# Kernel optimization log

Measured on AMD Instinct MI355X. Metric: run time of the kernel, lower is better.

Reference implementation:

```python
import jax, jax.numpy as jnp
import numpy as np

B, S, D, H = 2, 2048, 1024, 16
DK = D // H


def setup_inputs() -> dict:
    key = jax.random.key(0)
    ks = jax.random.split(key, 8)
    q = jax.random.normal(ks[0], (B, S, D), dtype=jnp.float32)
    k = jax.random.normal(ks[1], (B, S, D), dtype=jnp.float32)
    v = jax.random.normal(ks[2], (B, S, D), dtype=jnp.float32)
    mask = jax.random.randint(ks[3], (B, 1, S, S), 0, 2, dtype=jnp.int32)
    sc = 1.0 / np.sqrt(D)
    Wq = jax.random.normal(ks[4], (D, D), dtype=jnp.float32) * sc
    Wk = jax.random.normal(ks[5], (D, D), dtype=jnp.float32) * sc
    Wv = jax.random.normal(ks[6], (D, D), dtype=jnp.float32) * sc
    Wo = jax.random.normal(ks[7], (D, D), dtype=jnp.float32) * sc
    return {"q": q, "k": k, "v": v, "mask": mask, "Wq": Wq, "Wk": Wk, "Wv": Wv, "Wo": Wo}


def reference(q, k, v, mask, Wq, Wk, Wv, Wo):
    # Linear projections (torch Linear: x @ W.T; bias=False). Weights here stored
    # as [D, D] applied as x @ W (equivalent parameterization).
    query = q @ Wq  # [B,S,D]
    key = k @ Wk
    value = v @ Wv
    # split heads -> [B,H,S,DK]
    query = query.reshape(B, S, H, DK).transpose(0, 2, 1, 3)
    key = key.reshape(B, S, H, DK).transpose(0, 2, 1, 3)
    value = value.reshape(B, S, H, DK).transpose(0, 2, 1, 3)
    scores = jnp.einsum('bhqd,bhkd->bhqk', query, key) / jnp.sqrt(jnp.float32(DK))
    scores = jnp.where(mask == 0, jnp.float32(-1e9), scores)
    probs = jax.nn.softmax(scores, axis=-1)  # dropout p=0.0 -> identity
    x = jnp.einsum('bhqk,bhkd->bhqd', probs, value)
    x = x.transpose(0, 2, 1, 3).reshape(B, S, D)
    return x @ Wo
```

## Files before the change

### kernel.cpp

```cpp
#include <hip/hip_runtime.h>
#include <hip/hip_bf16.h>
#include <math.h>

#define B_ 2
#define S_ 2048
#define D_ 1024
#define H_ 16
#define DK_ 64
#define SW_ (S_ / 64)

typedef unsigned short u16;
typedef unsigned int u32;
typedef unsigned long long u64;
typedef __attribute__((ext_vector_type(8))) short short8;
typedef __attribute__((ext_vector_type(4))) float float4_;
typedef __attribute__((ext_vector_type(4))) unsigned int uint4_;

static __device__ inline u16 f_to_bf16(float f) {
    union { float f; u32 i; } x; x.f = f;
    u32 r = x.i + 0x7fff + ((x.i >> 16) & 1);
    return (u16)(r >> 16);
}

static __device__ __forceinline__ u32 cvtpk(float a, float b) {
    u32 r;
    asm("v_cvt_pk_bf16_f32 %0, %1, %2" : "=v"(r) : "v"(a), "v"(b));
    return r;
}

static __device__ __forceinline__ float fast_exp2(float x) {
#if __has_builtin(__builtin_amdgcn_exp2f)
    return __builtin_amdgcn_exp2f(x);
#else
    return exp2f(x);
#endif
}

static __device__ inline void gl_lds16(const u16* g, u16* l) {
    __builtin_amdgcn_global_load_lds((const __attribute__((address_space(1))) void*)g,
                                     (__attribute__((address_space(3))) void*)l, 16, 0, 0);
}

__global__ __launch_bounds__(256) void prep(const float* __restrict__ q,
                                            const float* __restrict__ k,
                                            const float* __restrict__ v,
                                            const int* __restrict__ mask,
                                            const float* __restrict__ W0,
                                            const float* __restrict__ W1,
                                            const float* __restrict__ W2,
                                            const float* __restrict__ W3,
                                            u16* __restrict__ qb, u16* __restrict__ kb,
                                            u16* __restrict__ vb,
                                            u16* __restrict__ T0, u16* __restrict__ T1,
                                            u16* __restrict__ T2, u16* __restrict__ T3,
                                            u64* __restrict__ mpk) {
    __shared__ float tile[32][33];
    int gx = blockIdx.x, tid = threadIdx.x;
    if (gx < 6144) {
        int z = gx >> 11;
        int bx = gx & 2047;
        const float* s = (z == 0) ? q : ((z == 1) ? k : v);
        u16* d = (z == 0) ? qb : ((z == 1) ? kb : vb);
        int i = (bx * 256 + tid) * 8;
        #pragma unroll
        for (int j = 0; j < 8; ++j) d[i + j] = f_to_bf16(s[i + j]);
    } else if (gx < 10240) {
        int g2 = gx - 6144;
        int z = g2 >> 10;
        int rem = g2 & 1023;
        const float* W = (z == 0) ? W0 : ((z == 1) ? W1 : ((z == 2) ? W2 : W3));
        u16* Wt = (z == 0) ? T0 : ((z == 1) ? T1 : ((z == 2) ? T2 : T3));
        int k0 = (rem >> 5) * 32, n0 = (rem & 31) * 32;
        int tx = tid & 31, ty = tid >> 5;
        #pragma unroll
        for (int i2 = 0; i2 < 4; ++i2) {
            int row = ty + i2 * 8;
            tile[row][tx] = W[(size_t)(k0 + row) * D_ + n0 + tx];
        }
        __syncthreads();
        #pragma unroll
        for (int i2 = 0; i2 < 4; ++i2) {
            int row = ty + i2 * 8;
            Wt[(size_t)(n0 + row) * D_ + k0 + tx] = f_to_bf16(tile[tx][row]);
        }
    } else {
        int g3 = gx - 10240;
        int wv = (g3 * 256 + tid) >> 6;
        int lane = tid & 63;
        #pragma unroll
        for (int i2 = 0; i2 < 8; ++i2) {
            int wd = wv * 8 + i2;
            u64 bits = __ballot(mask[(size_t)wd * 64 + lane] != 0);
            if (lane == 0) mpk[wd] = bits;
        }
    }
}

static __device__ __forceinline__ void gemm128_body(u16* lds,
                                                    const u16* __restrict__ A,
                                                    const u16* __restrict__ Bt,
                                                    int K, float4_ (&acc)[4][4]) {
    u16* ldsA = lds;
    u16* ldsB = lds + 8192;
    int tm = blockIdx.x, tn = blockIdx.y;
    int t = threadIdx.x, l = t & 63;
    int w = t >> 6, wr = w >> 1, wc = w & 1;
    int colL = l & 15, grp = l >> 4;
    int sw4 = (grp ^ ((colL >> 1) & 3)) << 3;
    int f0 = t, f1 = t + 256;
    int row0 = f0 >> 2, kc0 = (((f0 & 3) ^ ((f0 >> 3) & 3)) << 3);
    int row1 = f1 >> 2, kc1 = (((f1 & 3) ^ ((f1 >> 3) & 3)) << 3);
    const u16* gA0 = A  + (size_t)(tm * 128 + row0) * K + kc0;
    const u16* gA1 = A  + (size_t)(tm * 128 + row1) * K + kc1;
    const u16* gB0 = Bt + (size_t)(tn * 128 + row0) * K + kc0;
    const u16* gB1 = Bt + (size_t)(tn * 128 + row1) * K + kc1;

    #pragma unroll
    for (int mi = 0; mi < 4; ++mi)
        #pragma unroll
        for (int ni = 0; ni < 4; ++ni)
            acc[mi][ni] = (float4_){0.f, 0.f, 0.f, 0.f};

    gl_lds16(gA0, ldsA + f0 * 8);
    gl_lds16(gA1, ldsA + f1 * 8);
    gl_lds16(gB0, ldsB + f0 * 8);
    gl_lds16(gB1, ldsB + f1 * 8);

    for (int k0 = 0; k0 < K; k0 += 32) {
        int cur = (k0 >> 5) & 1;
        if (k0 + 32 < K) {
            int nb = (cur ^ 1) * 4096;
            gl_lds16(gA0 + k0 + 32, ldsA + nb + f0 * 8);
            gl_lds16(gA1 + k0 + 32, ldsA + nb + f1 * 8);
            gl_lds16(gB0 + k0 + 32, ldsB + nb + f0 * 8);
            gl_lds16(gB1 + k0 + 32, ldsB + nb + f1 * 8);
            asm volatile("s_waitcnt vmcnt(4)" ::: "memory");
        } else {
            asm volatile("s_waitcnt vmcnt(0)" ::: "memory");
        }
        __builtin_amdgcn_s_barrier();
        const u16* cA = ldsA + cur * 4096;
        const u16* cB = ldsB + cur * 4096;
        short8 a[4], b[4];
        #pragma unroll
        for (int mi = 0; mi < 4; ++mi)
            a[mi] = *(const short8*)&cA[(wr * 64 + mi * 16 + colL) * 32 + sw4];
        #pragma unroll
        for (int ni = 0; ni < 4; ++ni)
            b[ni] = *(const short8*)&cB[(wc * 64 + ni * 16 + colL) * 32 + sw4];
        #pragma unroll
        for (int mi = 0; mi < 4; ++mi)
            #pragma unroll
            for (int ni = 0; ni < 4; ++ni)
                acc[mi][ni] = __builtin_amdgcn_mfma_f32_16x16x32_bf16(a[mi], b[ni], acc[mi][ni], 0, 0, 0);
        __builtin_amdgcn_s_barrier();
    }
}

__global__ __launch_bounds__(256, 3) void gemm_qkv(const u16* __restrict__ qb,
                                                   const u16* __restrict__ kb,
                                                   const u16* __restrict__ vb,
                                                   const u16* __restrict__ Wqt,
                                                   const u16* __restrict__ Wkt,
                                                   const u16* __restrict__ Wvt,
                                                   u16* __restrict__ Qp,
                                                   u16* __restrict__ Kp,
                                                   u16* __restrict__ Vt) {
    __shared__ u16 lds[16384];
    int z = blockIdx.z;
    const u16* A  = (z == 0) ? qb  : ((z == 1) ? kb  : vb);
    const u16* Bt = (z == 0) ? Wqt : ((z == 1) ? Wkt : Wvt);
    float4_ acc[4][4];
    gemm128_body(lds, A, Bt, D_, acc);

    int tm = blockIdx.x, tn = blockIdx.y;
    int t = threadIdx.x, l = t & 63;
    int w = t >> 6, wr = w >> 1, wc = w & 1;
    int colL = l & 15, grp = l >> 4;

    if (z < 2) {
        u16* Y = (z == 0) ? Qp : Kp;
        float sc = (z == 0) ? (0.125f * 1.44269504f) : 1.0f;
        #pragma unroll
        for (int mi = 0; mi < 4; ++mi)
            #pragma unroll
            for (int ni = 0; ni < 4; ++ni)
                #pragma unroll
                for (int r = 0; r < 4; ++r)
                    Y[(size_t)(tm * 128 + wr * 64 + mi * 16 + grp * 4 + r) * D_
                      + tn * 128 + wc * 64 + ni * 16 + colL] = f_to_bf16(acc[mi][ni][r] * sc);
    } else {
        int tok_base = tm * 128 + wr * 64;
        int bb = tok_base >> 11;
        int s_hi = tok_base & (S_ - 1);
        #pragma unroll
        for (int mi = 0; mi < 4; ++mi)
            #pragma unroll
            for (int ni = 0; ni < 4; ++ni) {
                int n  = tn * 128 + wc * 64 + ni * 16 + colL;
                int hh = n >> 6, dk = n & 63;
                u16* vp = Vt + ((size_t)(bb * H_ + hh) * DK_ + dk) * S_ + s_hi;
                #pragma unroll
                for (int r = 0; r < 4; ++r) {
                    int m = mi * 16 + grp * 4 + r;
                    int mp_ = ((m >> 5) & 1) * 32 + ((m >> 2) & 3) * 8 + ((m >> 4) & 1) * 4 + (m & 3);
                    vp[mp_] = f_to_bf16(acc[mi][ni][r]);
                }
            }
    }
}

__global__ __launch_bounds__(256, 3) void gemm_out(const u16* __restrict__ Xa,
                                                   const u16* __restrict__ Wot,
                                                   float* __restrict__ out) {
    __shared__ u16 lds[16384];
    float4_ acc[4][4];
    gemm128_body(lds, Xa, Wot, D_, acc);

    int tm = blockIdx.x, tn = blockIdx.y;
    int t = threadIdx.x, l = t & 63;
    int w = t >> 6, wr = w >> 1, wc = w & 1;
    int colL = l & 15, grp = l >> 4;
    #pragma unroll
    for (int mi = 0; mi < 4; ++mi)
        #pragma unroll
        for (int ni = 0; ni < 4; ++ni)
            #pragma unroll
            for (int r = 0; r < 4; ++r)
                out[(size_t)(tm * 128 + wr * 64 + mi * 16 + grp * 4 + r) * D_
                    + tn * 128 + wc * 64 + ni * 16 + colL] = acc[mi][ni][r];
}

__global__ __launch_bounds__(256, 2) void attn128(const u16* __restrict__ Qp,
                                                  const u16* __restrict__ Kp,
                                                  const u16* __restrict__ Vt,
                                                  const u64* __restrict__ mp,
                                                  u16* __restrict__ Xa) {
    __shared__ u16 ldsK[2 * 128 * 64];
    __shared__ u16 ldsV[2 * 2 * 64 * 64];

    int bid0 = blockIdx.x;
    int bid = ((bid0 & 7) << 6) | (bid0 >> 3);
    int qt = bid & 15, h = (bid >> 4) & 15, b = bid >> 8;
    int t = threadIdx.x, l = t & 63, w = t >> 6;
    int colL = l & 15, grp = l >> 4;

    const u16* qbA = Qp + (size_t)(b * S_ + qt * 128 + w * 32 + colL) * D_ + h * DK_;
    const u16* qbB = qbA + (size_t)16 * D_;
    short8 qfA0 = *(const short8*)(qbA + grp * 8);
    short8 qfA1 = *(const short8*)(qbA + 32 + grp * 8);
    short8 qfB0 = *(const short8*)(qbB + grp * 8);
    short8 qfB1 = *(const short8*)(qbB + 32 + grp * 8);

    const u16* gK[4];
    const u16* gV[4];
    int fofs[4];
    #pragma unroll
    for (int i = 0; i < 4; ++i) {
        int f = t + 256 * i;
        fofs[i] = f * 8;
        int krow = f >> 3, kch = (((f & 7) ^ (krow & 7)) << 3);
        gK[i] = Kp + (size_t)(b * S_ + krow) * D_ + h * DK_ + kch;
        int hreg = f >> 9, fp = f & 511;
        int vrow = fp >> 3, vch = (((fp & 7) ^ (vrow & 7)) << 3);
        gV[i] = Vt + ((size_t)(b * H_ + h) * DK_ + vrow) * S_ + hreg * 64 + vch;
    }

    int sw8 = (grp ^ (colL & 7)) << 3;

    short8 onesb;
    #pragma unroll
    for (int j = 0; j < 8; ++j) onesb[j] = (short)0x3F80;

    float4_ laccA = (float4_){0.f, 0.f, 0.f, 0.f};
    float4_ laccB = (float4_){0.f, 0.f, 0.f, 0.f};
    float4_ oA[4], oB[4];
    #pragma unroll
    for (int nt = 0; nt < 4; ++nt) {
        oA[nt] = (float4_){0.f, 0.f, 0.f, 0.f};
        oB[nt] = (float4_){0.f, 0.f, 0.f, 0.f};
    }

    const u64* mrA = mp + (size_t)(b * S_ + qt * 128 + w * 32 + colL) * SW_;
    const u64* mrB = mrA + (size_t)16 * SW_;

    #pragma unroll
    for (int i = 0; i < 4; ++i) {
        gl_lds16(gK[i], ldsK + fofs[i]);
        gl_lds16(gV[i], ldsV + fofs[i]);
    }

    for (int kt = 0; kt < S_; kt += 128) {
        int cur = (kt >> 7) & 1;

        u64 mwA0 = mrA[(kt >> 6)];
        u64 mwA1 = mrA[(kt >> 6) + 1];
        u64 mwB0 = mrB[(kt >> 6)];
        u64 mwB1 = mrB[(kt >> 6) + 1];

        if (kt + 128 < S_) {
            int nb = (cur ^ 1) * 8192;
            #pragma unroll
            for (int i = 0; i < 4; ++i) {
                gl_lds16(gK[i] + (size_t)(kt + 128) * D_, ldsK + nb + fofs[i]);
                gl_lds16(gV[i] + (kt + 128),              ldsV + nb + fofs[i]);
            }
            asm volatile("s_waitcnt vmcnt(12)" ::: "memory");
        } else {
            asm volatile("s_waitcnt vmcnt(4)" ::: "memory");
        }
        __builtin_amdgcn_s_barrier();

        const u16* K_ = ldsK + cur * 8192;
        const u16* V_ = ldsV + cur * 8192;

        float4_ sA[8], sB[8];
        __builtin_amdgcn_s_setprio(1);
        #pragma unroll
        for (int nt = 0; nt < 8; ++nt) {
            int ro = (nt * 16 + colL) * 64;
            short8 kf0 = *(const short8*)&K_[ro + sw8];
            short8 kf1 = *(const short8*)&K_[ro + (sw8 ^ 32)];
            sA[nt] = (float4_){0.f, 0.f, 0.f, 0.f};
            sA[nt] = __builtin_amdgcn_mfma_f32_16x16x32_bf16(kf0, qfA0, sA[nt], 0, 0, 0);
            sA[nt] = __builtin_amdgcn_mfma_f32_16x16x32_bf16(kf1, qfA1, sA[nt], 0, 0, 0);
            sB[nt] = (float4_){0.f, 0.f, 0.f, 0.f};
            sB[nt] = __builtin_amdgcn_mfma_f32_16x16x32_bf16(kf0, qfB0, sB[nt], 0, 0, 0);
            sB[nt] = __builtin_amdgcn_mfma_f32_16x16x32_bf16(kf1, qfB1, sB[nt], 0, 0, 0);
        }
        __builtin_amdgcn_s_setprio(0);

        u64 mshA0 = mwA0 >> (grp * 4), mshA1 = mwA1 >> (grp * 4);
        u64 mshB0 = mwB0 >> (grp * 4), mshB1 = mwB1 >> (grp * 4);
        #pragma unroll
        for (int nt = 0; nt < 8; ++nt) {
            u32 bitsA = ((u32)((nt < 4 ? mshA0 : mshA1) >> ((nt & 3) * 16))) & 15u;
            u32 bitsB = ((u32)((nt < 4 ? mshB0 : mshB1) >> ((nt & 3) * 16))) & 15u;
            #pragma unroll
            for (int r = 0; r < 4; ++r) {
                float pA = fast_exp2(sA[nt][r]);
                float pB = fast_exp2(sB[nt][r]);
                u32 keepA = 0u - ((bitsA >> r) & 1u);
                u32 keepB = 0u - ((bitsB >> r) & 1u);
                union { float f; u32 i; } ua, ub;
                ua.f = pA; ua.i &= keepA; sA[nt][r] = ua.f;
                ub.f = pB; ub.i &= keepB; sB[nt][r] = ub.f;
            }
        }

        short8 pfA[4], pfB[4];
        #pragma unroll
        for (int j = 0; j < 4; ++j) {
            uint4_ Ax = { cvtpk(sA[2 * j][0], sA[2 * j][1]), cvtpk(sA[2 * j][2], sA[2 * j][3]),
                          cvtpk(sA[2 * j + 1][0], sA[2 * j + 1][1]), cvtpk(sA[2 * j + 1][2], sA[2 * j + 1][3]) };
            pfA[j] = __builtin_bit_cast(short8, Ax);
            uint4_ Bx = { cvtpk(sB[2 * j][0], sB[2 * j][1]), cvtpk(sB[2 * j][2], sB[2 * j][3]),
                          cvtpk(sB[2 * j + 1][0], sB[2 * j + 1][1]), cvtpk(sB[2 * j + 1][2], sB[2 * j + 1][3]) };
            pfB[j] = __builtin_bit_cast(short8, Bx);
        }

        __builtin_amdgcn_s_setprio(1);
        #pragma unroll
        for (int nt = 0; nt < 4; ++nt) {
            int ro = (nt * 16 + colL) * 64;
            short8 vf0 = *(const short8*)&V_[ro + sw8];
            short8 vf1 = *(const short8*)&V_[ro + (sw8 ^ 32)];
            short8 vf2 = *(const short8*)&V_[4096 + ro + sw8];
            short8 vf3 = *(const short8*)&V_[4096 + ro + (sw8 ^ 32)];
            oA[nt] = __builtin_amdgcn_mfma_f32_16x16x32_bf16(pfA[0], vf0, oA[nt], 0, 0, 0);
            oA[nt] = __builtin_amdgcn_mfma_f32_16x16x32_bf16(pfA[1], vf1, oA[nt], 0, 0, 0);
            oA[nt] = __builtin_amdgcn_mfma_f32_16x16x32_bf16(pfA[2], vf2, oA[nt], 0, 0, 0);
            oA[nt] = __builtin_amdgcn_mfma_f32_16x16x32_bf16(pfA[3], vf3, oA[nt], 0, 0, 0);
            oB[nt] = __builtin_amdgcn_mfma_f32_16x16x32_bf16(pfB[0], vf0, oB[nt], 0, 0, 0);
            oB[nt] = __builtin_amdgcn_mfma_f32_16x16x32_bf16(pfB[1], vf1, oB[nt], 0, 0, 0);
            oB[nt] = __builtin_amdgcn_mfma_f32_16x16x32_bf16(pfB[2], vf2, oB[nt], 0, 0, 0);
            oB[nt] = __builtin_amdgcn_mfma_f32_16x16x32_bf16(pfB[3], vf3, oB[nt], 0, 0, 0);
        }
        laccA = __builtin_amdgcn_mfma_f32_16x16x32_bf16(pfA[0], onesb, laccA, 0, 0, 0);
        laccA = __builtin_amdgcn_mfma_f32_16x16x32_bf16(pfA[1], onesb, laccA, 0, 0, 0);
        laccA = __builtin_amdgcn_mfma_f32_16x16x32_bf16(pfA[2], onesb, laccA, 0, 0, 0);
        laccA = __builtin_amdgcn_mfma_f32_16x16x32_bf16(pfA[3], onesb, laccA, 0, 0, 0);
        laccB = __builtin_amdgcn_mfma_f32_16x16x32_bf16(pfB[0], onesb, laccB, 0, 0, 0);
        laccB = __builtin_amdgcn_mfma_f32_16x16x32_bf16(pfB[1], onesb, laccB, 0, 0, 0);
        laccB = __builtin_amdgcn_mfma_f32_16x16x32_bf16(pfB[2], onesb, laccB, 0, 0, 0);
        laccB = __builtin_amdgcn_mfma_f32_16x16x32_bf16(pfB[3], onesb, laccB, 0, 0, 0);
        __builtin_amdgcn_s_setprio(0);

        __builtin_amdgcn_s_barrier();
    }

    float invA[4], invB[4];
    #pragma unroll
    for (int r = 0; r < 4; ++r) {
        invA[r] = 1.f / laccA[r];
        invB[r] = 1.f / laccB[r];
    }

    u16* xoA = Xa + (size_t)(b * S_ + qt * 128 + w * 32 + grp * 4) * D_ + h * DK_;
    u16* xoB = xoA + (size_t)16 * D_;
    #pragma unroll
    for (int r = 0; r < 4; ++r)
        #pragma unroll
        for (int nt = 0; nt < 4; ++nt) {
            xoA[(size_t)r * D_ + nt * 16 + colL] = f_to_bf16(oA[nt][r] * invA[r]);
            xoB[(size_t)r * D_ + nt * 16 + colL] = f_to_bf16(oB[nt][r] * invB[r]);
        }
}

extern "C" void kernel_launch(void* const* d_in, const int* in_sizes, int n_in,
                              void* d_out, int out_size, void* d_ws, size_t ws_size,
                              hipStream_t stream) {
    const float* q    = (const float*)d_in[0];
    const float* k    = (const float*)d_in[1];
    const float* v    = (const float*)d_in[2];
    const int*   mask = (const int*)d_in[3];
    const float* Wq   = (const float*)d_in[4];
    const float* Wk   = (const float*)d_in[5];
    const float* Wv   = (const float*)d_in[6];
    const float* Wo   = (const float*)d_in[7];
    float* out = (float*)d_out;

    const int NQ = B_ * S_ * D_;
    const int NW = D_ * D_;

    u16* qb  = (u16*)d_ws;
    u16* kb  = qb  + NQ;
    u16* vb  = kb  + NQ;
    u16* Wqt = vb  + NQ;
    u16* Wkt = Wqt + NW;
    u16* Wvt = Wkt + NW;
    u16* Wot = Wvt + NW;
    u16* Qp  = Wot + NW;
    u16* Kp  = Qp  + NQ;
    u16* Vt  = Kp  + NQ;
    u16* Xa  = Vt  + NQ;
    u64* mpk = (u64*)(Xa + NQ);

    dim3 cblk(256);
    prep<<<14336, cblk, 0, stream>>>(q, k, v, mask, Wq, Wk, Wv, Wo,
                                     qb, kb, vb, Wqt, Wkt, Wvt, Wot, mpk);

    const int M = B_ * S_;
    gemm_qkv<<<dim3(M / 128, D_ / 128, 3), cblk, 0, stream>>>(qb, kb, vb, Wqt, Wkt, Wvt, Qp, Kp, Vt);

    attn128<<<B_ * H_ * (S_ / 128), cblk, 0, stream>>>(Qp, Kp, Vt, mpk, Xa);

    gemm_out<<<dim3(M / 128, D_ / 128), cblk, 0, stream>>>(Xa, Wot, out);
}
```

Measured before the change: 238.5 us.

## Fuse fp32-to-bf16 input conversion into QKV GEMM and retile output GEMM

The separate prep pass that converted q, k and v to bf16 is removed. The QKV GEMM now loads fp32 activations directly into registers, rounds them to bf16 and writes them to LDS while the MFMAs for the current k-step run, which removes a full write and re-read of three activation tensors. The output GEMM is rewritten with 64-row tiles to launch twice as many blocks and improve occupancy over the 256-tile grid. The cost is register-mediated A loads with extra conversion ALU work and an lgkmcnt wait inside the GEMM loop, plus less B-tile reuse in the output GEMM.

```diff
diff --git a/kernel.cpp b/kernel.cpp
--- a/kernel.cpp
+++ b/kernel.cpp
@@ -22,6 +22,13 @@
     return (u16)(r >> 16);
 }
 
+static __device__ __forceinline__ u32 packrne(float a, float b) {
+    union { float f; u32 i; } xa, xb; xa.f = a; xb.f = b;
+    u32 lo = (xa.i + 0x7fff + ((xa.i >> 16) & 1)) >> 16;
+    u32 hi = (xb.i + 0x7fff + ((xb.i >> 16) & 1)) & 0xffff0000u;
+    return lo | hi;
+}
+
 static __device__ __forceinline__ u32 cvtpk(float a, float b) {
     u32 r;
     asm("v_cvt_pk_bf16_f32 %0, %1, %2" : "=v"(r) : "v"(a), "v"(b));
@@ -41,33 +48,19 @@
                                      (__attribute__((address_space(3))) void*)l, 16, 0, 0);
 }
 
-__global__ __launch_bounds__(256) void prep(const float* __restrict__ q,
-                                            const float* __restrict__ k,
-                                            const float* __restrict__ v,
-                                            const int* __restrict__ mask,
+__global__ __launch_bounds__(256) void prep(const int* __restrict__ mask,
                                             const float* __restrict__ W0,
                                             const float* __restrict__ W1,
                                             const float* __restrict__ W2,
                                             const float* __restrict__ W3,
-                                            u16* __restrict__ qb, u16* __restrict__ kb,
-                                            u16* __restrict__ vb,
                                             u16* __restrict__ T0, u16* __restrict__ T1,
                                             u16* __restrict__ T2, u16* __restrict__ T3,
                                             u64* __restrict__ mpk) {
     __shared__ float tile[32][33];
     int gx = blockIdx.x, tid = threadIdx.x;
-    if (gx < 6144) {
-        int z = gx >> 11;
-        int bx = gx & 2047;
-        const float* s = (z == 0) ? q : ((z == 1) ? k : v);
-        u16* d = (z == 0) ? qb : ((z == 1) ? kb : vb);
-        int i = (bx * 256 + tid) * 8;
-        #pragma unroll
-        for (int j = 0; j < 8; ++j) d[i + j] = f_to_bf16(s[i + j]);
-    } else if (gx < 10240) {
-        int g2 = gx - 6144;
-        int z = g2 >> 10;
-        int rem = g2 & 1023;
+    if (gx < 4096) {
+        int z = gx >> 10;
+        int rem = gx & 1023;
         const float* W = (z == 0) ? W0 : ((z == 1) ? W1 : ((z == 2) ? W2 : W3));
         u16* Wt = (z == 0) ? T0 : ((z == 1) ? T1 : ((z == 2) ? T2 : T3));
         int k0 = (rem >> 5) * 32, n0 = (rem & 31) * 32;
@@ -84,7 +77,7 @@
             Wt[(size_t)(n0 + row) * D_ + k0 + tx] = f_to_bf16(tile[tx][row]);
         }
     } else {
-        int g3 = gx - 10240;
+        int g3 = gx - 4096;
         int wv = (g3 * 256 + tid) >> 6;
         int lane = tid & 63;
         #pragma unroll
@@ -96,12 +89,20 @@
     }
 }
 
-static __device__ __forceinline__ void gemm128_body(u16* lds,
-                                                    const u16* __restrict__ A,
-                                                    const u16* __restrict__ Bt,
-                                                    int K, float4_ (&acc)[4][4]) {
-    u16* ldsA = lds;
-    u16* ldsB = lds + 8192;
+__global__ __launch_bounds__(256, 3) void gemm_qkv(const float* __restrict__ q,
+                                                   const float* __restrict__ k,
+                                                   const float* __restrict__ v,
+                                                   const u16* __restrict__ Wqt,
+                                                   const u16* __restrict__ Wkt,
+                                                   const u16* __restrict__ Wvt,
+                                                   u16* __restrict__ Qp,
+                                                   u16* __restrict__ Kp,
+                                                   u16* __restrict__ Vt) {
+    __shared__ u16 ldsA[2 * 4096];
+    __shared__ u16 ldsB[2 * 4096];
+    int z = blockIdx.z;
+    const float* A = (z == 0) ? q : ((z == 1) ? k : v);
+    const u16* Bt = (z == 0) ? Wqt : ((z == 1) ? Wkt : Wvt);
     int tm = blockIdx.x, tn = blockIdx.y;
     int t = threadIdx.x, l = t & 63;
     int w = t >> 6, wr = w >> 1, wc = w & 1;
@@ -110,35 +111,55 @@
     int f0 = t, f1 = t + 256;
     int row0 = f0 >> 2, kc0 = (((f0 & 3) ^ ((f0 >> 3) & 3)) << 3);
     int row1 = f1 >> 2, kc1 = (((f1 & 3) ^ ((f1 >> 3) & 3)) << 3);
-    const u16* gA0 = A  + (size_t)(tm * 128 + row0) * K + kc0;
-    const u16* gA1 = A  + (size_t)(tm * 128 + row1) * K + kc1;
-    const u16* gB0 = Bt + (size_t)(tn * 128 + row0) * K + kc0;
-    const u16* gB1 = Bt + (size_t)(tn * 128 + row1) * K + kc1;
-
+    const float* gA0 = A + (size_t)(tm * 128 + row0) * D_ + kc0;
+    const float* gA1 = A + (size_t)(tm * 128 + row1) * D_ + kc1;
+    const u16* gB0 = Bt + (size_t)(tn * 128 + row0) * D_ + kc0;
+    const u16* gB1 = Bt + (size_t)(tn * 128 + row1) * D_ + kc1;
+
+    float4_ acc[4][4];
     #pragma unroll
     for (int mi = 0; mi < 4; ++mi)
         #pragma unroll
         for (int ni = 0; ni < 4; ++ni)
             acc[mi][ni] = (float4_){0.f, 0.f, 0.f, 0.f};
 
-    gl_lds16(gA0, ldsA + f0 * 8);
-    gl_lds16(gA1, ldsA + f1 * 8);
     gl_lds16(gB0, ldsB + f0 * 8);
     gl_lds16(gB1, ldsB + f1 * 8);
-
-    for (int k0 = 0; k0 < K; k0 += 32) {
+    {
+        float4_ a0 = *(const float4_*)(gA0);
+        float4_ a1 = *(const float4_*)(gA0 + 4);
+        float4_ a2 = *(const float4_*)(gA1);
+        float4_ a3 = *(const float4_*)(gA1 + 4);
+        uint4_ w0 = { packrne(a0[0], a0[1]), packrne(a0[2], a0[3]),
+                      packrne(a1[0], a1[1]), packrne(a1[2], a1[3]) };
+        uint4_ w1 = { packrne(a2[0], a2[1]), packrne(a2[2], a2[3]),
+                      packrne(a3[0], a3[1]), packrne(a3[2], a3[3]) };
+        *(uint4_*)(ldsA + f0 * 8) = w0;
+        *(uint4_*)(ldsA + f1 * 8) = w1;
+    }
+
+    for (int k0 = 0; k0 < D_; k0 += 32) {
         int cur = (k0 >> 5) & 1;
-        if (k0 + 32 < K) {
-            int nb = (cur ^ 1) * 4096;
-            gl_lds16(gA0 + k0 + 32, ldsA + nb + f0 * 8);
-            gl_lds16(gA1 + k0 + 32, ldsA + nb + f1 * 8);
+        int nb = (cur ^ 1) * 4096;
+        bool more = (k0 + 32 < D_);
+        if (more) {
             gl_lds16(gB0 + k0 + 32, ldsB + nb + f0 * 8);
             gl_lds16(gB1 + k0 + 32, ldsB + nb + f1 * 8);
-            asm volatile("s_waitcnt vmcnt(4)" ::: "memory");
+            asm volatile("s_waitcnt vmcnt(2)" ::: "memory");
         } else {
             asm volatile("s_waitcnt vmcnt(0)" ::: "memory");
         }
-        __builtin_amdgcn_s_barrier();
+        asm volatile("s_waitcnt lgkmcnt(0)" ::: "memory");
+        __builtin_amdgcn_s_barrier();
+
+        float4_ a0, a1, a2, a3;
+        if (more) {
+            a0 = *(const float4_*)(gA0 + k0 + 32);
+            a1 = *(const float4_*)(gA0 + k0 + 36);
+            a2 = *(const float4_*)(gA1 + k0 + 32);
+            a3 = *(const float4_*)(gA1 + k0 + 36);
+        }
+
         const u16* cA = ldsA + cur * 4096;
         const u16* cB = ldsB + cur * 4096;
         short8 a[4], b[4];
@@ -153,30 +174,17 @@
             #pragma unroll
             for (int ni = 0; ni < 4; ++ni)
                 acc[mi][ni] = __builtin_amdgcn_mfma_f32_16x16x32_bf16(a[mi], b[ni], acc[mi][ni], 0, 0, 0);
-        __builtin_amdgcn_s_barrier();
-    }
-}
-
-__global__ __launch_bounds__(256, 3) void gemm_qkv(const u16* __restrict__ qb,
-                                                   const u16* __restrict__ kb,
-                                                   const u16* __restrict__ vb,
-                                                   const u16* __restrict__ Wqt,
-                                                   const u16* __restrict__ Wkt,
-                                                   const u16* __restrict__ Wvt,
-                                                   u16* __restrict__ Qp,
-                                                   u16* __restrict__ Kp,
-                                                   u16* __restrict__ Vt) {
-    __shared__ u16 lds[16384];
-    int z = blockIdx.z;
-    const u16* A  = (z == 0) ? qb  : ((z == 1) ? kb  : vb);
-    const u16* Bt = (z == 0) ? Wqt : ((z == 1) ? Wkt : Wvt);
-    float4_ acc[4][4];
-    gemm128_body(lds, A, Bt, D_, acc);
-
-    int tm = blockIdx.x, tn = blockIdx.y;
-    int t = threadIdx.x, l = t & 63;
-    int w = t >> 6, wr = w >> 1, wc = w & 1;
-    int colL = l & 15, grp = l >> 4;
+
+        if (more) {
+            uint4_ w0 = { packrne(a0[0], a0[1]), packrne(a0[2], a0[3]),
+                          packrne(a1[0], a1[1]), packrne(a1[2], a1[3]) };
+            uint4_ w1 = { packrne(a2[0], a2[1]), packrne(a2[2], a2[3]),
+                          packrne(a3[0], a3[1]), packrne(a3[2], a3[3]) };
+            *(uint4_*)(ldsA + nb + f0 * 8) = w0;
+            *(uint4_*)(ldsA + nb + f1 * 8) = w1;
+        }
+        __builtin_amdgcn_s_barrier();
+    }
 
     if (z < 2) {
         u16* Y = (z == 0) ? Qp : Kp;
@@ -210,24 +218,69 @@
     }
 }
 
-__global__ __launch_bounds__(256, 3) void gemm_out(const u16* __restrict__ Xa,
+__global__ __launch_bounds__(256, 2) void gemm_out(const u16* __restrict__ Xa,
                                                    const u16* __restrict__ Wot,
                                                    float* __restrict__ out) {
-    __shared__ u16 lds[16384];
-    float4_ acc[4][4];
-    gemm128_body(lds, Xa, Wot, D_, acc);
-
+    __shared__ u16 ldsA[2 * 2048];
+    __shared__ u16 ldsB[2 * 4096];
     int tm = blockIdx.x, tn = blockIdx.y;
     int t = threadIdx.x, l = t & 63;
     int w = t >> 6, wr = w >> 1, wc = w & 1;
     int colL = l & 15, grp = l >> 4;
-    #pragma unroll
-    for (int mi = 0; mi < 4; ++mi)
+    int sw4 = (grp ^ ((colL >> 1) & 3)) << 3;
+    int f0 = t, f1 = t + 256;
+    int row0 = f0 >> 2, kc0 = (((f0 & 3) ^ ((f0 >> 3) & 3)) << 3);
+    int row1 = f1 >> 2, kc1 = (((f1 & 3) ^ ((f1 >> 3) & 3)) << 3);
+    const u16* gA0 = Xa  + (size_t)(tm * 64 + row0) * D_ + kc0;
+    const u16* gB0 = Wot + (size_t)(tn * 128 + row0) * D_ + kc0;
+    const u16* gB1 = Wot + (size_t)(tn * 128 + row1) * D_ + kc1;
+
+    float4_ acc[2][4];
+    #pragma unroll
+    for (int mi = 0; mi < 2; ++mi)
         #pragma unroll
         for (int ni = 0; ni < 4; ++ni)
+            acc[mi][ni] = (float4_){0.f, 0.f, 0.f, 0.f};
+
+    gl_lds16(gA0, ldsA + f0 * 8);
+    gl_lds16(gB0, ldsB + f0 * 8);
+    gl_lds16(gB1, ldsB + f1 * 8);
+
+    for (int k0 = 0; k0 < D_; k0 += 32) {
+        int cur = (k0 >> 5) & 1;
+        if (k0 + 32 < D_) {
+            gl_lds16(gA0 + k0 + 32, ldsA + (cur ^ 1) * 2048 + f0 * 8);
+            gl_lds16(gB0 + k0 + 32, ldsB + (cur ^ 1) * 4096 + f0 * 8);
+            gl_lds16(gB1 + k0 + 32, ldsB + (cur ^ 1) * 4096 + f1 * 8);
+            asm volatile("s_waitcnt vmcnt(3)" ::: "memory");
+        } else {
+            asm volatile("s_waitcnt vmcnt(0)" ::: "memory");
+        }
+        __builtin_amdgcn_s_barrier();
+        const u16* cA = ldsA + cur * 2048;
+        const u16* cB = ldsB + cur * 4096;
+        short8 a[2], b[4];
+        #pragma unroll
+        for (int mi = 0; mi < 2; ++mi)
+            a[mi] = *(const short8*)&cA[(wr * 32 + mi * 16 + colL) * 32 + sw4];
+        #pragma unroll
+        for (int ni = 0; ni < 4; ++ni)
+            b[ni] = *(const short8*)&cB[(wc * 64 + ni * 16 + colL) * 32 + sw4];
+        #pragma unroll
+        for (int mi = 0; mi < 2; ++mi)
+            #pragma unroll
+            for (int ni = 0; ni < 4; ++ni)
+                acc[mi][ni] = __builtin_amdgcn_mfma_f32_16x16x32_bf16(a[mi], b[ni], acc[mi][ni], 0, 0, 0);
+        __builtin_amdgcn_s_barrier();
+    }
+
+    #pragma unroll
+    for (int mi = 0; mi < 2; ++mi)
+        #pragma unroll
+        for (int ni = 0; ni < 4; ++ni)
             #pragma unroll
             for (int r = 0; r < 4; ++r)
-                out[(size_t)(tm * 128 + wr * 64 + mi * 16 + grp * 4 + r) * D_
+                out[(size_t)(tm * 64 + wr * 32 + mi * 16 + grp * 4 + r) * D_
                     + tn * 128 + wc * 64 + ni * 16 + colL] = acc[mi][ni][r];
 }
 
@@ -423,10 +476,7 @@
     const int NQ = B_ * S_ * D_;
     const int NW = D_ * D_;
 
-    u16* qb  = (u16*)d_ws;
-    u16* kb  = qb  + NQ;
-    u16* vb  = kb  + NQ;
-    u16* Wqt = vb  + NQ;
+    u16* Wqt = (u16*)d_ws;
     u16* Wkt = Wqt + NW;
     u16* Wvt = Wkt + NW;
     u16* Wot = Wvt + NW;
@@ -437,13 +487,13 @@
     u64* mpk = (u64*)(Xa + NQ);
 
     dim3 cblk(256);
-    prep<<<14336, cblk, 0, stream>>>(q, k, v, mask, Wq, Wk, Wv, Wo,
-                                     qb, kb, vb, Wqt, Wkt, Wvt, Wot, mpk);
+    prep<<<8192, cblk, 0, stream>>>(mask, Wq, Wk, Wv, Wo,
+                                    Wqt, Wkt, Wvt, Wot, mpk);
 
     const int M = B_ * S_;
-    gemm_qkv<<<dim3(M / 128, D_ / 128, 3), cblk, 0, stream>>>(qb, kb, vb, Wqt, Wkt, Wvt, Qp, Kp, Vt);
+    gemm_qkv<<<dim3(M / 128, D_ / 128, 3), cblk, 0, stream>>>(q, k, v, Wqt, Wkt, Wvt, Qp, Kp, Vt);
 
     attn128<<<B_ * H_ * (S_ / 128), cblk, 0, stream>>>(Qp, Kp, Vt, mpk, Xa);
 
-    gemm_out<<<dim3(M / 128, D_ / 128), cblk, 0, stream>>>(Xa, Wot, out);
-}
+    gemm_out<<<dim3(M / 64, D_ / 128), cblk, 0, stream>>>(Xa, Wot, out);
+}
```

Measured after the change: 259.6 us. +8.8%, slower.
